# Performance work log

Measured on AMD Instinct MI355X. Metric: run time of the kernel, lower is better.

Reference implementation:

```python
import jax, jax.numpy as jnp
import numpy as np

N_NODES = 100000
N_EDGES = 1600000
D_IN, D_HID, N_CLS, N_LAYERS = 128, 256, 10, 3


def setup_inputs() -> dict:
    key = jax.random.key(0)
    ks = jax.random.split(key, 8)
    x = jax.random.normal(ks[0], (N_NODES, D_IN), dtype=jnp.float32)
    edge_index = jax.random.randint(ks[1], (2, N_EDGES), 0, N_NODES, dtype=jnp.int64)
    s = 0.05
    Wl = jax.random.normal(ks[2], (N_LAYERS, D_HID, D_IN), dtype=jnp.float32) * s
    Wr = jax.random.normal(ks[3], (N_LAYERS, D_HID, D_IN), dtype=jnp.float32) * s
    bias = jnp.zeros((N_LAYERS, D_HID), dtype=jnp.float32)
    W1 = jax.random.normal(ks[4], (D_HID, D_HID), dtype=jnp.float32) * s
    b1 = jnp.zeros((D_HID,), dtype=jnp.float32)
    W2 = jax.random.normal(ks[5], (N_CLS, D_HID), dtype=jnp.float32) * s
    b2 = jnp.zeros((N_CLS,), dtype=jnp.float32)
    return {"x": x, "edge_index": edge_index, "Wl": Wl, "Wr": Wr, "bias": bias,
            "W1": W1, "b1": b1, "W2": W2, "b2": b2}


def reference(x, edge_index, Wl, Wr, bias, W1, b1, W2, b2):
    n = x.shape[0]
    src, tgt = edge_index[0], edge_index[1]
    # mean aggregation of source-node features onto targets (SAGEConv aggr='mean')
    deg = jax.ops.segment_sum(jnp.ones(src.shape[0], x.dtype), tgt, num_segments=n)
    agg = jax.ops.segment_sum(x[src], tgt, num_segments=n)  # [N, D_in]
    agg = agg / jnp.clip(deg, 1.0)[:, None]
    # Every layer consumes the ORIGINAL x (per the source forward), so agg is shared.
    h = None
    for l in range(Wl.shape[0]):
        h = jax.nn.relu(agg @ Wl[l].T + x @ Wr[l].T + bias[l])  # [N, D_hid]
    # global_mean_pool over all nodes (single graph)
    pooled = jnp.mean(h, axis=0, keepdims=True)  # [1, D_hid]
    z = jax.nn.relu(pooled @ W1.T + b1)
    z = z @ W2.T + b2
    return jax.nn.log_softmax(z, axis=1)
```

## Files before the change

kernel.cpp:

```cpp
#include <hip/hip_runtime.h>
#include <hip/hip_bf16.h>

#define D_IN  128
#define D_HID 256
#define CBITS 7
#define CSIZE 128
#define EPB   8192
#define CCAP  4096

typedef __bf16 bf16x8 __attribute__((ext_vector_type(8)));
typedef float  f32x4  __attribute__((ext_vector_type(4)));
typedef float  f32x2  __attribute__((ext_vector_type(2)));

__device__ __forceinline__ unsigned short f2bf(float f) {
    unsigned u = __float_as_uint(f);
    u += 0x7FFFu + ((u >> 16) & 1u);
    return (unsigned short)(u >> 16);
}
__device__ __forceinline__ uint2 pack4(float4 v) {
    unsigned lo = (unsigned)f2bf(v.x) | ((unsigned)f2bf(v.y) << 16);
    unsigned hi = (unsigned)f2bf(v.z) | ((unsigned)f2bf(v.w) << 16);
    return make_uint2(lo, hi);
}
__device__ __forceinline__ unsigned packfp8(float4 v) {
    int u = __builtin_amdgcn_cvt_pk_fp8_f32(v.x, v.y, 0, false);
    u = __builtin_amdgcn_cvt_pk_fp8_f32(v.z, v.w, u, true);
    return (unsigned)u;
}
__device__ __forceinline__ void g2lds16(const void* g, void* l) {
    __builtin_amdgcn_global_load_lds(
        (const __attribute__((address_space(1))) unsigned int*)g,
        (__attribute__((address_space(3))) unsigned int*)l, 16, 0, 0);
}
__device__ __forceinline__ void acc8(f32x2& a0, f32x2& a1, f32x2& a2, f32x2& a3, uint2 v) {
    a0 += __builtin_amdgcn_cvt_pk_f32_fp8(v.x, false);
    a1 += __builtin_amdgcn_cvt_pk_f32_fp8(v.x, true);
    a2 += __builtin_amdgcn_cvt_pk_f32_fp8(v.y, false);
    a3 += __builtin_amdgcn_cvt_pk_f32_fp8(v.y, true);
}

__global__ __launch_bounds__(256)
void prep(const float* __restrict__ x, unsigned short* __restrict__ xb,
          unsigned char* __restrict__ x8,
          const float* __restrict__ Wr2, const float* __restrict__ Wl2,
          unsigned short* __restrict__ Bsw,
          int* __restrict__ gcur, float* __restrict__ pooled_pad,
          long n16, int NXB, int NCB) {
    const int bid = blockIdx.x;
    const int tid = threadIdx.x;
    if (bid < NXB) {
        const long t = (long)bid * 256 + tid;
        if (t >= n16) return;
        const float4* x4 = (const float4*)x;
        float4 v0 = x4[t * 4], v1 = x4[t * 4 + 1], v2 = x4[t * 4 + 2], v3 = x4[t * 4 + 3];
        uint2 p0 = pack4(v0), p1 = pack4(v1), p2 = pack4(v2), p3 = pack4(v3);
        ((uint4*)xb)[t * 2]     = make_uint4(p0.x, p0.y, p1.x, p1.y);
        ((uint4*)xb)[t * 2 + 1] = make_uint4(p2.x, p2.y, p3.x, p3.y);
        ((uint4*)x8)[t] = make_uint4(packfp8(v0), packfp8(v1), packfp8(v2), packfp8(v3));
    } else if (bid < NXB + 32) {
        const int t_idx = (bid - NXB) * 256 + tid;
        const int lane = t_idx & 63;
        const int rest = t_idx >> 6;
        const int tt   = rest & 3;
        const int wn2  = (rest >> 2) & 3;
        const int kk   = rest >> 4;
        const int j = wn2 * 64 + tt * 16 + (lane & 15);
        const int k = kk * 32 + (lane >> 4) * 8;
        const float* src = (k < 128) ? &Wr2[j * 128 + k] : &Wl2[j * 128 + (k - 128)];
        float4 v0 = *(const float4*)src;
        float4 v1 = *(const float4*)(src + 4);
        uint2 p0 = pack4(v0), p1 = pack4(v1);
        *(uint4*)&Bsw[(long)t_idx * 8] = make_uint4(p0.x, p0.y, p1.x, p1.y);
    } else {
        for (int i = tid; i < NCB * 16; i += 256) gcur[i] = 0;
        for (int i = tid; i < 256 * 16; i += 256) pooled_pad[i] = 0.f;
    }
}

__global__ __launch_bounds__(256)
void coarse_bin(const void* __restrict__ ei, int* __restrict__ gcur,
                unsigned* __restrict__ segc, int E, int NCB) {
    __shared__ int cnt[1024];
    __shared__ int basel[1024];
    __shared__ int s_is64;
    const int tid = threadIdx.x;
    const long e0 = (long)blockIdx.x * EPB;
    const int ecnt = (int)min((long)EPB, (long)E - e0);

    if (tid < 64) {
        const int v = ((const int*)ei)[2 * tid + 1];
        const unsigned long long b = __ballot(v != 0);
        if (tid == 0) s_is64 = (b == 0ull);
    }
    for (int i = tid; i < NCB; i += 256) cnt[i] = 0;
    __syncthreads();
    const int is64 = s_is64;

    for (int j = tid; j < ecnt; j += 256) {
        int t = is64 ? (int)((const long long*)ei)[E + e0 + j]
                     : ((const int*)ei)[E + e0 + j];
        atomicAdd(&cnt[t >> CBITS], 1);
    }
    __syncthreads();

    for (int c = tid; c < NCB; c += 256) {
        const int n = cnt[c];
        const int na = (n + 15) & ~15;
        int b = 0;
        if (na > 0) b = atomicAdd(&gcur[c * 16], na);
        basel[c] = b;
        cnt[c] = 0;
        unsigned* sp = segc + (long)c * CCAP;
        for (int i = n; i < na; ++i)
            if (b + i < CCAP) sp[b + i] = 0xFFFFFFFFu;
    }
    __syncthreads();

    for (int j = tid; j < ecnt; j += 256) {
        int s, t;
        if (is64) { const long long* p = (const long long*)ei; s = (int)p[e0 + j]; t = (int)p[E + e0 + j]; }
        else      { const int* p = (const int*)ei;             s = p[e0 + j];      t = p[E + e0 + j]; }
        const int c = t >> CBITS;
        const int r = atomicAdd(&cnt[c], 1);
        const int pos = basel[c] + r;
        if (pos < CCAP)
            segc[(long)c * CCAP + pos] = ((unsigned)s << CBITS) | (unsigned)(t & (CSIZE - 1));
    }
}

__global__ __launch_bounds__(512)
void refine_gather(const int* __restrict__ gcur, const unsigned* __restrict__ segc,
                   const unsigned char* __restrict__ x8,
                   unsigned short* __restrict__ aggb, int M) {
    __shared__ unsigned order[CCAP];
    __shared__ int degh[CSIZE], scn[CSIZE], cur[CSIZE];
    const int tid = threadIdx.x;
    const int cb = blockIdx.x;
    const int nbase = cb << CBITS;
    const int nn = min(CSIZE, M - nbase);
    const int len = min(gcur[cb * 16], CCAP);
    const unsigned* sp = segc + (long)cb * CCAP;

    if (tid < CSIZE) degh[tid] = 0;
    __syncthreads();
    for (int i = tid; i < len; i += 512) {
        const unsigned e = sp[i];
        if (e != 0xFFFFFFFFu) atomicAdd(&degh[e & (CSIZE - 1)], 1);
    }
    __syncthreads();
    if (tid < CSIZE) scn[tid] = degh[tid];
    __syncthreads();
    for (int off = 1; off < CSIZE; off <<= 1) {
        int v = 0;
        if (tid >= off && tid < CSIZE) v = scn[tid - off];
        __syncthreads();
        if (tid < CSIZE) scn[tid] += v;
        __syncthreads();
    }
    if (tid < CSIZE) cur[tid] = scn[tid] - degh[tid];
    __syncthreads();
    for (int i = tid; i < len; i += 512) {
        const unsigned e = sp[i];
        if (e != 0xFFFFFFFFu) {
            const int r = atomicAdd(&cur[e & (CSIZE - 1)], 1);
            order[r] = e & ~(unsigned)(CSIZE - 1);
        }
    }
    __syncthreads();

    const int lane = tid & 63;
    const int wave = tid >> 6;
    const int ns   = lane >> 4;
    const int c2   = lane & 15;
    const unsigned chb = (unsigned)c2 * 8;

    for (int base = wave * 4; base < nn; base += 32) {
        const int nl = base + ns;
        int deg = 0, beg = 0;
        if (nl < nn) { deg = degh[nl]; beg = scn[nl] - deg; }
        f32x2 a0 = {0.f, 0.f}, a1 = {0.f, 0.f}, a2 = {0.f, 0.f}, a3 = {0.f, 0.f};
        int i = 0;
        for (; i + 2 <= deg; i += 2) {
            const unsigned o0 = order[beg + i];
            const unsigned o1 = order[beg + i + 1];
            uint2 v0 = *(const uint2*)(x8 + (o0 + chb));
            uint2 v1 = *(const uint2*)(x8 + (o1 + chb));
            acc8(a0, a1, a2, a3, v0);
            acc8(a0, a1, a2, a3, v1);
        }
        if (i < deg) {
            const unsigned o0 = order[beg + i];
            uint2 v0 = *(const uint2*)(x8 + (o0 + chb));
            acc8(a0, a1, a2, a3, v0);
        }
        if (nl < nn) {
            const float rdiv = 1.0f / fmaxf((float)deg, 1.0f);
            unsigned w0 = (unsigned)f2bf(a0.x * rdiv) | ((unsigned)f2bf(a0.y * rdiv) << 16);
            unsigned w1 = (unsigned)f2bf(a1.x * rdiv) | ((unsigned)f2bf(a1.y * rdiv) << 16);
            unsigned w2 = (unsigned)f2bf(a2.x * rdiv) | ((unsigned)f2bf(a2.y * rdiv) << 16);
            unsigned w3 = (unsigned)f2bf(a3.x * rdiv) | ((unsigned)f2bf(a3.y * rdiv) << 16);
            *(uint4*)(aggb + (long)(nbase + nl) * 128 + c2 * 8) = make_uint4(w0, w1, w2, w3);
        }
    }
}

__global__ __launch_bounds__(256, 2)
void gemm_pool(const unsigned short* __restrict__ xb, const unsigned short* __restrict__ aggb,
               const unsigned short* __restrict__ Bsw, const float* __restrict__ bias2,
               float* __restrict__ pooled_pad, int M, int NT) {
    __shared__ unsigned short As[4 * 32 * 256];
    const int tid  = threadIdx.x;
    const int lane = tid & 63;
    const int wn2  = tid >> 6;
    const int lrow = lane & 15;
    const int quad = lane >> 4;
    const int bid  = blockIdx.x;
    const int GRID = gridDim.x;
    const int nt   = (NT - bid + GRID - 1) / GRID;
    if (nt <= 0) return;

    uint4 bb[8][4];
    #pragma unroll
    for (int kk = 0; kk < 8; ++kk)
        #pragma unroll
        for (int t = 0; t < 4; ++t)
            bb[kk][t] = *(const uint4*)&Bsw[((((long)kk * 4 + wn2) * 4 + t) * 64 + lane) * 8];
    float bv[4];
    #pragma unroll
    for (int t = 0; t < 4; ++t) bv[t] = bias2[wn2 * 64 + t * 16 + lrow];

    const int cl = tid & 31;
    const int rw = tid >> 5;
    const int cs = cl ^ rw;
    const unsigned short* sbase = (cs < 16) ? (xb + (long)cs * 8)
                                            : (aggb + (long)(cs - 16) * 8);
    char* lbase = (char*)As + rw * 512 + cl * 16;

    auto STAGE = [&](int p) {
        const long trow = ((long)bid + (long)p * GRID) * 32;
        char* ld = lbase + (p & 3) * 16384;
        #pragma unroll
        for (int s = 0; s < 4; ++s)
            g2lds16(sbase + (trow + s * 8 + rw) * 128, ld + s * 4096);
    };

    #pragma unroll
    for (int p = 0; p < 3; ++p) if (p < nt) STAGE(p);

    float ps[4] = {0.f, 0.f, 0.f, 0.f};

    for (int p = 0; p < nt; ++p) {
        const int rem = nt - 1 - p;
        if (rem >= 2)      asm volatile("s_waitcnt vmcnt(8)" ::: "memory");
        else if (rem == 1) asm volatile("s_waitcnt vmcnt(4)" ::: "memory");
        else               asm volatile("s_waitcnt vmcnt(0)" ::: "memory");
        __builtin_amdgcn_s_barrier();
        if (p + 3 < nt) STAGE(p + 3);

        const char* Ab = (const char*)As + (p & 3) * 16384;
        f32x4 acc[2][4] = {};
        #pragma unroll
        for (int kk = 0; kk < 8; ++kk) {
            uint4 aC[2];
            #pragma unroll
            for (int i = 0; i < 2; ++i) {
                const int r = i * 16 + lrow;
                aC[i] = *(const uint4*)(Ab + r * 512 + (((kk * 4 + quad) ^ (lrow & 7)) * 16));
            }
            #pragma unroll
            for (int i = 0; i < 2; ++i)
                #pragma unroll
                for (int t = 0; t < 4; ++t)
                    acc[i][t] = __builtin_amdgcn_mfma_f32_16x16x32_bf16(
                        *(bf16x8*)&aC[i], *(bf16x8*)&bb[kk][t], acc[i][t], 0, 0, 0);
        }

        const long trow = ((long)bid + (long)p * GRID) * 32;
        #pragma unroll
        for (int t = 0; t < 4; ++t) {
            float s = 0.f;
            #pragma unroll
            for (int i = 0; i < 2; ++i) {
                const long rbase = trow + i * 16 + quad * 4;
                #pragma unroll
                for (int r = 0; r < 4; ++r) {
                    float h = fmaxf(acc[i][t][r] + bv[t], 0.f);
                    if (rbase + r < M) s += h;
                }
            }
            ps[t] += s;
        }
    }

    #pragma unroll
    for (int t = 0; t < 4; ++t) {
        ps[t] += __shfl_xor(ps[t], 16);
        ps[t] += __shfl_xor(ps[t], 32);
        if (quad == 0)
            atomicAdd(&pooled_pad[(wn2 * 64 + t * 16 + lrow) * 16], ps[t]);
    }
}

__global__ __launch_bounds__(256)
void head_kernel(const float* __restrict__ pooled_pad,
                 const float* __restrict__ W1, const float* __restrict__ b1,
                 const float* __restrict__ W2, const float* __restrict__ b2,
                 float* __restrict__ out, float invM) {
    __shared__ float pooled_s[256];
    __shared__ float z1_s[256];
    __shared__ float z2_s[10];
    const int j = threadIdx.x;

    pooled_s[j] = pooled_pad[j * 16] * invM;
    __syncthreads();

    const float4* w4 = (const float4*)(W1 + (long)j * 256);
    float sx = 0.f, sy = 0.f, sz = 0.f, sw = 0.f;
    #pragma unroll 8
    for (int k = 0; k < 64; ++k) {
        float4 w = w4[k];
        float4 p = *(const float4*)&pooled_s[k * 4];
        sx += w.x * p.x; sy += w.y * p.y; sz += w.z * p.z; sw += w.w * p.w;
    }
    z1_s[j] = fmaxf(b1[j] + sx + sy + sz + sw, 0.f);
    __syncthreads();

    if (j < 160) {
        const int c = j >> 4, q = j & 15;
        float s = 0.f;
        for (int k = q; k < 256; k += 16) s += W2[c * 256 + k] * z1_s[k];
        #pragma unroll
        for (int off = 8; off >= 1; off >>= 1) s += __shfl_down(s, off, 16);
        if (q == 0) z2_s[c] = s + b2[c];
    }
    __syncthreads();

    if (j == 0) {
        float mx = z2_s[0];
        for (int c = 1; c < 10; ++c) mx = fmaxf(mx, z2_s[c]);
        float se = 0.f;
        for (int c = 0; c < 10; ++c) se += expf(z2_s[c] - mx);
        const float ls = logf(se);
        for (int c = 0; c < 10; ++c) out[c] = z2_s[c] - mx - ls;
    }
}

extern "C" void kernel_launch(void* const* d_in, const int* in_sizes, int n_in,
                              void* d_out, int out_size, void* d_ws, size_t ws_size,
                              hipStream_t stream) {
    const float* x    = (const float*)d_in[0];
    const void*  ei   = d_in[1];
    const float* Wl   = (const float*)d_in[2];
    const float* Wr   = (const float*)d_in[3];
    const float* bias = (const float*)d_in[4];
    const float* W1   = (const float*)d_in[5];
    const float* b1   = (const float*)d_in[6];
    const float* W2   = (const float*)d_in[7];
    const float* b2   = (const float*)d_in[8];
    float* out = (float*)d_out;

    const int M = in_sizes[0] / D_IN;
    const int E = in_sizes[1] / 2;
    const int L = in_sizes[4] / D_HID;
    const int NMB = (M + 127) / 128;
    const long Mpad = (long)NMB * 128;
    const int NCB = (M + CSIZE - 1) / CSIZE;
    const int NB1 = (E + EPB - 1) / EPB;
    const int NT  = (M + 31) / 32;
    const int NG  = (NT < 512) ? NT : 512;

    const float* Wl2   = Wl + (long)(L - 1) * D_HID * D_IN;
    const float* Wr2   = Wr + (long)(L - 1) * D_HID * D_IN;
    const float* bias2 = bias + (long)(L - 1) * D_HID;

    unsigned short* xb   = (unsigned short*)d_ws;
    unsigned short* aggb = xb + Mpad * D_IN;
    unsigned char*  x8   = (unsigned char*)(aggb + Mpad * D_IN);
    unsigned short* Bsw  = (unsigned short*)(x8 + Mpad * D_IN);
    float* pooled_pad    = (float*)(Bsw + 256 * 256);
    int*      gcur       = (int*)(pooled_pad + 256 * 16);
    unsigned* segc       = (unsigned*)(gcur + (long)NCB * 16);

    const long n16 = (long)M * 8;
    const int NXB = (int)((n16 + 255) / 256);

    prep<<<NXB + 32 + 1, 256, 0, stream>>>(x, xb, x8, Wr2, Wl2, Bsw, gcur, pooled_pad,
                                           n16, NXB, NCB);
    coarse_bin<<<NB1, 256, 0, stream>>>(ei, gcur, segc, E, NCB);
    refine_gather<<<NCB, 512, 0, stream>>>(gcur, segc, x8, aggb, M);

    gemm_pool<<<NG, 256, 0, stream>>>(xb, aggb, Bsw, bias2, pooled_pad, M, NT);

    head_kernel<<<1, 256, 0, stream>>>(pooled_pad, W1, b1, W2, b2, out, 1.0f / (float)M);
}
```

Before: 235.2 us.

## Locally counting-sort edges in LDS before coalesced coarse-bin scatter

The coarse binning kernel now reads each edge once into registers, counts per bucket, and runs an LDS prefix scan. It then counting-sorts the packed edges into shared memory and writes each bucket's run to global memory in contiguous order. This replaces the second global read of the edge list and the scattered per-edge global writes. It also halves edges per block, doubles threads per block, and drops the 16-entry sentinel padding of bucket segments, which downstream code may have relied on.

```diff
diff --git a/kernel.cpp b/kernel.cpp
--- a/kernel.cpp
+++ b/kernel.cpp
@@ -5,7 +5,7 @@
 #define D_HID 256
 #define CBITS 7
 #define CSIZE 128
-#define EPB   8192
+#define EPB   4096
 #define CCAP  4096
 
 typedef __bf16 bf16x8 __attribute__((ext_vector_type(8)));
@@ -77,11 +77,12 @@
     }
 }
 
-__global__ __launch_bounds__(256)
+__global__ __launch_bounds__(512)
 void coarse_bin(const void* __restrict__ ei, int* __restrict__ gcur,
                 unsigned* __restrict__ segc, int E, int NCB) {
-    __shared__ int cnt[1024];
-    __shared__ int basel[1024];
+    __shared__ unsigned sorted[EPB];
+    __shared__ unsigned short bkt[EPB];
+    __shared__ int cnt[1024], scn[1024], cur[1024], gbase[1024];
     __shared__ int s_is64;
     const int tid = threadIdx.x;
     const long e0 = (long)blockIdx.x * EPB;
@@ -92,39 +93,60 @@
         const unsigned long long b = __ballot(v != 0);
         if (tid == 0) s_is64 = (b == 0ull);
     }
-    for (int i = tid; i < NCB; i += 256) cnt[i] = 0;
+    for (int i = tid; i < 1024; i += 512) cnt[i] = 0;
     __syncthreads();
     const int is64 = s_is64;
 
-    for (int j = tid; j < ecnt; j += 256) {
-        int t = is64 ? (int)((const long long*)ei)[E + e0 + j]
-                     : ((const int*)ei)[E + e0 + j];
-        atomicAdd(&cnt[t >> CBITS], 1);
-    }
-    __syncthreads();
-
-    for (int c = tid; c < NCB; c += 256) {
-        const int n = cnt[c];
-        const int na = (n + 15) & ~15;
-        int b = 0;
-        if (na > 0) b = atomicAdd(&gcur[c * 16], na);
-        basel[c] = b;
-        cnt[c] = 0;
-        unsigned* sp = segc + (long)c * CCAP;
-        for (int i = n; i < na; ++i)
-            if (b + i < CCAP) sp[b + i] = 0xFFFFFFFFu;
-    }
-    __syncthreads();
-
-    for (int j = tid; j < ecnt; j += 256) {
-        int s, t;
-        if (is64) { const long long* p = (const long long*)ei; s = (int)p[e0 + j]; t = (int)p[E + e0 + j]; }
-        else      { const int* p = (const int*)ei;             s = p[e0 + j];      t = p[E + e0 + j]; }
-        const int c = t >> CBITS;
-        const int r = atomicAdd(&cnt[c], 1);
-        const int pos = basel[c] + r;
-        if (pos < CCAP)
-            segc[(long)c * CCAP + pos] = ((unsigned)s << CBITS) | (unsigned)(t & (CSIZE - 1));
+    int sv[8], tv[8];
+    #pragma unroll
+    for (int k = 0; k < 8; ++k) {
+        const int j = tid + k * 512;
+        if (j < ecnt) {
+            if (is64) {
+                sv[k] = (int)((const long long*)ei)[e0 + j];
+                tv[k] = (int)((const long long*)ei)[E + e0 + j];
+            } else {
+                sv[k] = ((const int*)ei)[e0 + j];
+                tv[k] = ((const int*)ei)[E + e0 + j];
+            }
+            atomicAdd(&cnt[tv[k] >> CBITS], 1);
+        }
+    }
+    __syncthreads();
+
+    scn[tid] = cnt[tid];
+    scn[tid + 512] = cnt[tid + 512];
+    __syncthreads();
+    for (int off = 1; off < 1024; off <<= 1) {
+        const int v0 = (tid >= off) ? scn[tid - off] : 0;
+        const int v1 = (tid + 512 >= off) ? scn[tid + 512 - off] : 0;
+        __syncthreads();
+        scn[tid] += v0;
+        scn[tid + 512] += v1;
+        __syncthreads();
+    }
+    cur[tid] = scn[tid] - cnt[tid];
+    cur[tid + 512] = scn[tid + 512] - cnt[tid + 512];
+    for (int c = tid; c < NCB; c += 512)
+        gbase[c] = cnt[c] ? atomicAdd(&gcur[c * 16], cnt[c]) : 0;
+    __syncthreads();
+
+    #pragma unroll
+    for (int k = 0; k < 8; ++k) {
+        const int j = tid + k * 512;
+        if (j < ecnt) {
+            const int c = tv[k] >> CBITS;
+            const int r = atomicAdd(&cur[c], 1);
+            sorted[r] = ((unsigned)sv[k] << CBITS) | (unsigned)(tv[k] & (CSIZE - 1));
+            bkt[r] = (unsigned short)c;
+        }
+    }
+    __syncthreads();
+
+    for (int i = tid; i < ecnt; i += 512) {
+        const int c = bkt[i];
+        const int pos = gbase[c] + (i - (scn[c] - cnt[c]));
+        if (pos < CCAP) segc[(long)c * CCAP + pos] = sorted[i];
     }
 }
 
@@ -386,7 +408,7 @@
 
     prep<<<NXB + 32 + 1, 256, 0, stream>>>(x, xb, x8, Wr2, Wl2, Bsw, gcur, pooled_pad,
                                            n16, NXB, NCB);
-    coarse_bin<<<NB1, 256, 0, stream>>>(ei, gcur, segc, E, NCB);
+    coarse_bin<<<NB1, 512, 0, stream>>>(ei, gcur, segc, E, NCB);
     refine_gather<<<NCB, 512, 0, stream>>>(gcur, segc, x8, aggb, M);
 
     gemm_pool<<<NG, 256, 0, stream>>>(xb, aggb, Bsw, bias2, pooled_pad, M, NT);
```

Result: faster. 214.3 us (-8.9%).
